# Optimization experiments

Hardware: AMD Instinct MI355X
Metric: run time of the kernel (lower is better)

## Reference

```python
import jax, jax.numpy as jnp
import numpy as np

B, S, D, H = 2, 2048, 1024, 16  # batch, seq, d_model, num_heads
DH = D // H


def setup_inputs() -> dict:
    key = jax.random.key(0)
    ks = jax.random.split(key, 11)
    sc = 1.0 / np.sqrt(D)
    return {
        "q": jax.random.normal(ks[0], (B, S, D), jnp.float32),
        "k": jax.random.normal(ks[1], (B, S, D), jnp.float32),
        "v": jax.random.normal(ks[2], (B, S, D), jnp.float32),
        "wq": jax.random.normal(ks[3], (D, D), jnp.float32) * sc,
        "bq": jax.random.normal(ks[4], (D,), jnp.float32) * 0.01,
        "wk": jax.random.normal(ks[5], (D, D), jnp.float32) * sc,
        "bk": jax.random.normal(ks[6], (D,), jnp.float32) * 0.01,
        "wv": jax.random.normal(ks[7], (D, D), jnp.float32) * sc,
        "bv": jax.random.normal(ks[8], (D,), jnp.float32) * 0.01,
        "wo": jax.random.normal(ks[9], (D, D), jnp.float32) * sc,
        "bo": jax.random.normal(ks[10], (D,), jnp.float32) * 0.01,
    }


def reference(q, k, v, wq, bq, wk, bk, wv, bv, wo, bo):
    # projections: [B,S,D]
    query = q @ wq + bq
    key_ = k @ wk + bk
    value = v @ wv + bv
    # split heads: [B,H,S,DH]
    def split(x):
        return jnp.transpose(x.reshape(B, S, H, DH), (0, 2, 1, 3))
    query, key_, value = split(query), split(key_), split(value)
    # NOTE: original module applies NO 1/sqrt(d_k) scaling
    scores = jnp.einsum("bhqd,bhkd->bhqk", query, key_)
    attn = jax.nn.softmax(scores, axis=-1)
    data = jnp.einsum("bhqk,bhkd->bhqd", attn, value)  # [B,H,S,DH]
    # faithful to original bug: transpose(0,1) then view(B,S,-1)
    data = jnp.swapaxes(data, 0, 1).reshape(B, S, D)
    return data @ wo + bo
```

## Files before the change

kernel.cpp:

```cpp
#include <hip/hip_runtime.h>

typedef _Float16 f16;
typedef _Float16 f16x8 __attribute__((ext_vector_type(8)));
typedef _Float16 f16x4 __attribute__((ext_vector_type(4)));
typedef __fp16   h16x2 __attribute__((ext_vector_type(2)));
typedef float    f32x4 __attribute__((ext_vector_type(4)));

static constexpr int BATCH = 2, SEQ = 2048, DMODEL = 1024, HEADS = 16, DHEAD = 64;
static constexpr int MTOK = BATCH * SEQ;
static constexpr float LOG2E = 1.44269504088896f;

#define GLOBAL_LOAD_LDS16(gptr, lptr)                                              \
  __builtin_amdgcn_global_load_lds(                                                \
      (const __attribute__((address_space(1))) void*)(gptr),                       \
      (__attribute__((address_space(3))) void*)(lptr), 16, 0, 0)

#define MFMA16(a, b, c) __builtin_amdgcn_mfma_f32_16x16x32_f16((a), (b), (c), 0, 0, 0)

#define WAITV_(N) asm volatile("s_waitcnt vmcnt(" #N ")" ::: "memory")
#define WAITV(N) WAITV_(N)

__device__ __forceinline__ float fexp2(float x) {
  float r;
  asm volatile("v_exp_f32 %0, %1" : "=v"(r) : "v"(x));
  return r;
}
__device__ __forceinline__ float m3(float a, float b, float c) {
  return fmaxf(fmaxf(a, b), c);
}

__device__ __forceinline__ int imgAB(int mr, int kr) {
  int pr = mr >> 1;
  int jj = ((mr & 1) << 2) | (kr >> 3);
  int j = jj ^ (pr & 7);
  return pr * 64 + j * 8 + (kr & 7);
}
__device__ __forceinline__ int imgK(int sr, int dh) {
  return sr * 64 + (((dh >> 3) ^ (sr & 7)) << 3) + (dh & 7);
}

__global__ __launch_bounds__(256) void cast3_kernel(
    const float* __restrict__ qs, const float* __restrict__ ks,
    const float* __restrict__ vs, f16* __restrict__ X0, f16* __restrict__ X1,
    f16* __restrict__ X2) {
  const int z = blockIdx.z;
  const float* src = z == 0 ? qs : z == 1 ? ks : vs;
  f16* dst = z == 0 ? X0 : z == 1 ? X1 : X2;
  int c = blockIdx.x * 256 + threadIdx.x;
  int blk = c >> 8, cb = c & 255;
  int pr = cb >> 3, j = cb & 7;
  int jj = j ^ (pr & 7);
  int mr = (pr << 1) | (jj >> 2);
  int kr = (jj & 3) << 3;
  int m = (blk >> 5) * 64 + mr;
  int k = (blk & 31) * 32 + kr;
  const float* s = src + (size_t)m * DMODEL + k;
  f32x4 a = *(const f32x4*)s, b = *(const f32x4*)(s + 4);
  f16x8 o;
  o[0] = (f16)a[0]; o[1] = (f16)a[1]; o[2] = (f16)a[2]; o[3] = (f16)a[3];
  o[4] = (f16)b[0]; o[5] = (f16)b[1]; o[6] = (f16)b[2]; o[7] = (f16)b[3];
  *(f16x8*)(dst + (size_t)c * 8) = o;
}

__global__ __launch_bounds__(256) void transw_kernel(
    const float* __restrict__ w0, const float* __restrict__ w1,
    const float* __restrict__ w2, const float* __restrict__ w3,
    f16* __restrict__ Wimg) {
  const int z = blockIdx.z;
  const float* w = z == 0 ? w0 : z == 1 ? w1 : z == 2 ? w2 : w3;
  f16* t = Wimg + (size_t)z * DMODEL * DMODEL;
  __shared__ f16 lt[64][72];
  const int k0 = blockIdx.x * 64, n0 = blockIdx.y * 64;
  const int r = threadIdx.x >> 2, c0 = (threadIdx.x & 3) * 16;
  const float* src = w + (size_t)(k0 + r) * DMODEL + n0 + c0;
#pragma unroll
  for (int jx = 0; jx < 16; jx += 4) {
    f32x4 x = *(const f32x4*)(src + jx);
    lt[c0 + jx + 0][r] = (f16)x[0];
    lt[c0 + jx + 1][r] = (f16)x[1];
    lt[c0 + jx + 2][r] = (f16)x[2];
    lt[c0 + jx + 3][r] = (f16)x[3];
  }
  __syncthreads();
  const int n = n0 + r;
#pragma unroll
  for (int cw = 0; cw < 2; cw++) {
    int k = k0 + c0 + cw * 8;
    int blk = ((n >> 6) << 5) | (k >> 5);
    int off = blk * 2048 + imgAB(n & 63, k & 31);
    f16x8 v;
#pragma unroll
    for (int e = 0; e < 8; e++) v[e] = lt[r][c0 + cw * 8 + e];
    *(f16x8*)(t + off) = v;
  }
}

__global__ __launch_bounds__(256) void proj_kernel(
    const f16* __restrict__ Ximg, const f16* __restrict__ Wimg,
    const float* __restrict__ bq, const float* __restrict__ bk,
    const float* __restrict__ bv, f16* __restrict__ Qp, f16* __restrict__ Kp,
    f16* __restrict__ Vt, int zbase, size_t aStride) {
  __shared__ f16 As[2][4096];
  __shared__ f16 Bs[2][4096];
  const int z = zbase + blockIdx.z;
  const f16* A = Ximg + (size_t)blockIdx.z * aStride;
  const f16* Bw = Wimg + (size_t)z * DMODEL * DMODEL;
  int lin = blockIdx.x + (blockIdx.y << 3);
  int swz = ((lin & 7) << 5) + (lin >> 3);
  const int n0 = (swz & 7) * 128, m0 = (swz >> 3) * 128;
  const int tid = threadIdx.x, w = tid >> 6, l = tid & 63, q = l & 15, g = l >> 4;
  const int wr = w >> 1, wc = w & 1;
  const int KT = DMODEL >> 5;
  int aoff[4], boff[4];
#pragma unroll
  for (int mi = 0; mi < 4; mi++) {
    int mr = wr * 64 + mi * 16 + q;
    aoff[mi] = ((mr >> 6) << 11) + imgAB(mr & 63, g * 8);
  }
#pragma unroll
  for (int ni = 0; ni < 4; ni++) {
    int nr = wc * 64 + ni * 16 + q;
    boff[ni] = ((nr >> 6) << 11) + imgAB(nr & 63, g * 8);
  }
  f32x4 acc[4][4] = {};

#define PROJ_STAGE(bb, t)                                                          \
  {                                                                                \
    _Pragma("unroll")                                                              \
    for (int i = 0; i < 2; i++) {                                                  \
      int c = w * 2 + i;                                                           \
      size_t ga = (size_t)(((m0 >> 6) + (c >> 2)) * KT + (t)) * 2048 +             \
                  (c & 3) * 512 + l * 8;                                           \
      GLOBAL_LOAD_LDS16(A + ga, (char*)&As[bb][c * 512]);                          \
      size_t gb = (size_t)(((n0 >> 6) + (c >> 2)) * KT + (t)) * 2048 +             \
                  (c & 3) * 512 + l * 8;                                           \
      GLOBAL_LOAD_LDS16(Bw + gb, (char*)&Bs[bb][c * 512]);                         \
    }                                                                              \
  }

  PROJ_STAGE(0, 0);
  for (int t = 0; t < KT; t++) {
    const int bb = t & 1;
    if (t < KT - 1) {
      PROJ_STAGE(bb ^ 1, t + 1);
      WAITV(4);
    } else {
      WAITV(0);
    }
    __builtin_amdgcn_s_barrier();
    f16x8 af[4], bf[4];
#pragma unroll
    for (int mi = 0; mi < 4; mi++) af[mi] = *(const f16x8*)&As[bb][aoff[mi]];
#pragma unroll
    for (int ni = 0; ni < 4; ni++) bf[ni] = *(const f16x8*)&Bs[bb][boff[ni]];
#pragma unroll
    for (int mi = 0; mi < 4; mi++)
#pragma unroll
      for (int ni = 0; ni < 4; ni++)
        acc[mi][ni] = MFMA16(af[mi], bf[ni], acc[mi][ni]);
    __builtin_amdgcn_s_barrier();
  }
  const float* bias = z == 0 ? bq : (z == 1 ? bk : bv);
#pragma unroll
  for (int mi = 0; mi < 4; mi++)
#pragma unroll
    for (int ni = 0; ni < 4; ni++) {
      const int col = n0 + wc * 64 + ni * 16 + q;
      const float bvl = bias[col];
      const int row0 = m0 + wr * 64 + mi * 16 + g * 4;
      if (z == 0) {
#pragma unroll
        for (int r = 0; r < 4; r++)
          Qp[(size_t)(row0 + r) * DMODEL + col] = (f16)((acc[mi][ni][r] + bvl) * LOG2E);
      } else if (z == 1) {
        const int h = col >> 6, dh = col & 63;
#pragma unroll
        for (int r = 0; r < 4; r++) {
          const int row = row0 + r, s = row & (SEQ - 1);
          Kp[(size_t)(((row >> 11) * HEADS + h) * 64 + (s >> 5)) * 2048 + imgK(s & 31, dh)] =
              (f16)(acc[mi][ni][r] + bvl);
        }
      } else {
        const int h = col >> 6, dh = col & 63;
        const int s0 = row0 & (SEQ - 1);
        f16* dst = Vt + (size_t)(((row0 >> 11) * HEADS + h) * 64 + (s0 >> 5)) * 2048 +
                   imgAB(dh, s0 & 31);
        f16x4 ov;
        ov[0] = (f16)(acc[mi][ni][0] + bvl); ov[1] = (f16)(acc[mi][ni][1] + bvl);
        ov[2] = (f16)(acc[mi][ni][2] + bvl); ov[3] = (f16)(acc[mi][ni][3] + bvl);
        *(f16x4*)dst = ov;
      }
    }
}

__global__ __launch_bounds__(128, 2) void attn_kernel(
    const f16* __restrict__ Qp, const f16* __restrict__ Kimg,
    const f16* __restrict__ Vimg, f16* __restrict__ Simg) {
  __shared__ f16 Klds[2][2][2048];
  __shared__ f16 Vlds[2][2][2048];
  __shared__ f16 Plds[2][2][2][512];
  const int tid = threadIdx.x, w = tid >> 6, l = tid & 63, q = l & 15, g = l >> 4;
  const int lin = blockIdx.x;
  const int swz = ((lin & 7) << 7) + (lin >> 3);
  const int qb = swz & 31, bh = swz >> 5;
  const int b = bh >> 4, h = bh & 15;
  const int q0 = qb * 64 + w * 32;

  const f16* qrowA = Qp + (size_t)(b * SEQ + q0 + q) * DMODEL + h * 64;
  const f16x8 qA0 = *(const f16x8*)(qrowA + g * 8);
  const f16x8 qA1 = *(const f16x8*)(qrowA + 32 + g * 8);
  const f16* qrowB = qrowA + (size_t)16 * DMODEL;
  const f16x8 qB0 = *(const f16x8*)(qrowB + g * 8);
  const f16x8 qB1 = *(const f16x8*)(qrowB + 32 + g * 8);

  const f16* kt_base = Kimg + (size_t)(bh * 64) * 2048;
  const f16* vt_base = Vimg + (size_t)(bh * 64) * 2048;

  int koff[4][2];
#pragma unroll
  for (int fn = 0; fn < 4; fn++)
#pragma unroll
    for (int hf = 0; hf < 2; hf++)
      koff[fn][hf] = (fn >> 1) * 2048 + imgK((fn & 1) * 16 + q, hf * 32 + g * 8);
  int voff[4];
#pragma unroll
  for (int fo = 0; fo < 4; fo++) voff[fo] = imgAB(fo * 16 + q, g * 8);
  const int poff = imgAB(q, g * 8);
  int pwoff[2];
  {
    const int pr = q >> 1;
#pragma unroll
    for (int fn = 0; fn < 2; fn++) {
      int jj = ((q & 1) << 2) | (fn * 2 + (g >> 1));
      pwoff[fn] = pr * 64 + ((jj ^ (pr & 7)) << 3) + (g & 1) * 4;
    }
  }
  f16* PwA = &Plds[w][0][0][0];
  f16* PwB = &Plds[w][1][0][0];
  float mA = -1.0e30f, mB = -1.0e30f, lA = 0.f, lB = 0.f;
  f32x4 oA[4] = {}, oB[4] = {};

#define ATTN_STAGE(bb, t)                                                          \
  {                                                                                \
    const f16* sb_ = (w == 0) ? (kt_base + (size_t)(2 * (t)) * 2048)               \
                              : (vt_base + (size_t)(2 * (t)) * 2048);              \
    f16* db_ = (w == 0) ? &Klds[bb][0][0] : &Vlds[bb][0][0];                       \
    _Pragma("unroll")                                                              \
    for (int j_ = 0; j_ < 8; j_++)                                                 \
      GLOBAL_LOAD_LDS16(sb_ + j_ * 512 + l * 8, (char*)(db_ + j_ * 512));          \
  }

#define SOFTMAX_FRAG(s, m_st, l_pt, o, PbF)                                        \
  {                                                                                \
    float lm = fmaxf(m3(m3(s[0][0], s[0][1], s[0][2]),                             \
                        m3(s[0][3], s[1][0], s[1][1]),                             \
                        m3(s[1][2], s[1][3], s[2][0])),                            \
                     m3(m3(s[2][1], s[2][2], s[2][3]),                             \
                        m3(s[3][0], s[3][1], s[3][2]), s[3][3]));                  \
    if (!__all(lm <= m_st + 8.f)) {                                                \
      float mx = fmaxf(lm, __shfl_xor(lm, 16, 64));                                \
      mx = fmaxf(mx, __shfl_xor(mx, 32, 64));                                      \
      const float mnew = fmaxf(m_st, mx);                                          \
      const float sc = fexp2(m_st - mnew);                                         \
      m_st = mnew;                                                                 \
      l_pt *= sc;                                                                  \
      _Pragma("unroll")                                                            \
      for (int fo_ = 0; fo_ < 4; fo_++) {                                          \
        o[fo_][0] *= sc; o[fo_][1] *= sc; o[fo_][2] *= sc; o[fo_][3] *= sc;        \
      }                                                                            \
    }                                                                              \
    float ts = 0.f;                                                                \
    _Pragma("unroll")                                                              \
    for (int fn_ = 0; fn_ < 4; fn_++) {                                            \
      float e0 = fexp2(s[fn_][0] - m_st);                                          \
      float e1 = fexp2(s[fn_][1] - m_st);                                          \
      float e2 = fexp2(s[fn_][2] - m_st);                                          \
      float e3 = fexp2(s[fn_][3] - m_st);                                          \
      ts += (e0 + e1) + (e2 + e3);                                                 \
      union { f16x4 v4; h16x2 h2[2]; } pu_;                                        \
      pu_.h2[0] = __builtin_amdgcn_cvt_pkrtz(e0, e1);                              \
      pu_.h2[1] = __builtin_amdgcn_cvt_pkrtz(e2, e3);                              \
      *(f16x4*)((PbF) + (fn_ >> 1) * 512 + pwoff[fn_ & 1]) = pu_.v4;               \
    }                                                                              \
    l_pt += ts;                                                                    \
  }

  ATTN_STAGE(0, 0);
  for (int t = 0; t < 32; t++) {
    const int bb = t & 1;
    if (t < 31) {
      ATTN_STAGE(bb ^ 1, t + 1);
      WAITV(8);
    } else {
      WAITV(0);
    }
    __builtin_amdgcn_s_barrier();
    const f16* Kb = &Klds[bb][0][0];
    f16x8 kf[4][2];
#pragma unroll
    for (int fn = 0; fn < 4; fn++) {
      kf[fn][0] = *(const f16x8*)(Kb + koff[fn][0]);
      kf[fn][1] = *(const f16x8*)(Kb + koff[fn][1]);
    }
    f32x4 sA[4], sB[4];
    __builtin_amdgcn_s_setprio(1);
#pragma unroll
    for (int fn = 0; fn < 4; fn++) {
      f32x4 z0 = {};
      z0 = MFMA16(kf[fn][0], qA0, z0);
      z0 = MFMA16(kf[fn][1], qA1, z0);
      sA[fn] = z0;
      f32x4 z1 = {};
      z1 = MFMA16(kf[fn][0], qB0, z1);
      z1 = MFMA16(kf[fn][1], qB1, z1);
      sB[fn] = z1;
    }
    __builtin_amdgcn_s_setprio(0);
    SOFTMAX_FRAG(sA, mA, lA, oA, PwA);
    SOFTMAX_FRAG(sB, mB, lB, oB, PwB);
    const f16x8 pA0 = *(const f16x8*)(PwA + poff);
    const f16x8 pA1 = *(const f16x8*)(PwA + 512 + poff);
    const f16x8 pB0 = *(const f16x8*)(PwB + poff);
    const f16x8 pB1 = *(const f16x8*)(PwB + 512 + poff);
    const f16* Vb = &Vlds[bb][0][0];
    f16x8 vf[4][2];
#pragma unroll
    for (int fo = 0; fo < 4; fo++) {
      vf[fo][0] = *(const f16x8*)(Vb + voff[fo]);
      vf[fo][1] = *(const f16x8*)(Vb + 2048 + voff[fo]);
    }
    __builtin_amdgcn_s_setprio(1);
#pragma unroll
    for (int fo = 0; fo < 4; fo++) {
      oA[fo] = MFMA16(vf[fo][0], pA0, oA[fo]);
      oA[fo] = MFMA16(vf[fo][1], pA1, oA[fo]);
      oB[fo] = MFMA16(vf[fo][0], pB0, oB[fo]);
      oB[fo] = MFMA16(vf[fo][1], pB1, oB[fo]);
    }
    __builtin_amdgcn_s_setprio(0);
    __builtin_amdgcn_s_barrier();
  }
  float lsA = lA + __shfl_xor(lA, 16, 64);
  lsA += __shfl_xor(lsA, 32, 64);
  float lsB = lB + __shfl_xor(lB, 16, 64);
  lsB += __shfl_xor(lsB, 32, 64);
  const float invA = 1.f / lsA, invB = 1.f / lsB;
  const int m16 = (2 * h + b) & 15, bp = h >> 3;
#pragma unroll
  for (int half = 0; half < 2; half++) {
    const int s = q0 + half * 16 + q;
    const int tp = bp * SEQ + m16 * 128 + (s >> 4);
    const float inv = half ? invB : invA;
    const f32x4* o = half ? oB : oA;
#pragma unroll
    for (int fo = 0; fo < 4; fo++) {
      const int d0 = (s & 15) * 64 + fo * 16 + g * 4;
      f16* dst = Simg + (size_t)(((tp >> 6) << 5) | (d0 >> 5)) * 2048 + imgAB(tp & 63, d0 & 31);
      f16x4 ov;
      ov[0] = (f16)(o[fo][0] * inv); ov[1] = (f16)(o[fo][1] * inv);
      ov[2] = (f16)(o[fo][2] * inv); ov[3] = (f16)(o[fo][3] * inv);
      *(f16x4*)dst = ov;
    }
  }
}

__global__ __launch_bounds__(256) void ogemm_kernel(
    const f16* __restrict__ Aimg, const f16* __restrict__ Bimg,
    const float* __restrict__ bias, float* __restrict__ out) {
  __shared__ f16 As[2][4096];
  __shared__ f16 Bs[2][2048];
  int lin = blockIdx.x + (blockIdx.y << 4);
  int swz = ((lin & 7) << 6) + (lin >> 3);
  const int n0 = (swz & 15) * 64, m0 = (swz >> 4) * 128;
  const int tid = threadIdx.x, w = tid >> 6, l = tid & 63, q = l & 15, g = l >> 4;
  const int wr = w >> 1, wc = w & 1;
  int aoff[4], boff[2];
#pragma unroll
  for (int mi = 0; mi < 4; mi++) {
    int mr = wr * 64 + mi * 16 + q;
    aoff[mi] = ((mr >> 6) << 11) + imgAB(mr & 63, g * 8);
  }
#pragma unroll
  for (int ni = 0; ni < 2; ni++) boff[ni] = imgAB(wc * 32 + ni * 16 + q, g * 8);
  f32x4 acc[4][2] = {};

#define OG_STAGE(bb, t)                                                            \
  {                                                                                \
    _Pragma("unroll")                                                              \
    for (int i = 0; i < 2; i++) {                                                  \
      int c = w * 2 + i;                                                           \
      size_t ga = (size_t)(((m0 >> 6) + (c >> 2)) * 32 + (t)) * 2048 +             \
                  (c & 3) * 512 + l * 8;                                           \
      GLOBAL_LOAD_LDS16(Aimg + ga, (char*)&As[bb][c * 512]);                       \
    }                                                                              \
    size_t gb = (size_t)((n0 >> 6) * 32 + (t)) * 2048 + w * 512 + l * 8;           \
    GLOBAL_LOAD_LDS16(Bimg + gb, (char*)&Bs[bb][w * 512]);                         \
  }

  OG_STAGE(0, 0);
  for (int t = 0; t < 32; t++) {
    const int bb = t & 1;
    if (t < 31) {
      OG_STAGE(bb ^ 1, t + 1);
      WAITV(3);
    } else {
      WAITV(0);
    }
    __builtin_amdgcn_s_barrier();
    f16x8 af[4], bf[2];
#pragma unroll
    for (int mi = 0; mi < 4; mi++) af[mi] = *(const f16x8*)&As[bb][aoff[mi]];
#pragma unroll
    for (int ni = 0; ni < 2; ni++) bf[ni] = *(const f16x8*)&Bs[bb][boff[ni]];
#pragma unroll
    for (int mi = 0; mi < 4; mi++)
#pragma unroll
      for (int ni = 0; ni < 2; ni++)
        acc[mi][ni] = MFMA16(af[mi], bf[ni], acc[mi][ni]);
    __builtin_amdgcn_s_barrier();
  }
#pragma unroll
  for (int mi = 0; mi < 4; mi++)
#pragma unroll
    for (int ni = 0; ni < 2; ni++) {
      const int col = n0 + wc * 32 + ni * 16 + q;
      const float bvl = bias[col];
      const int row0 = m0 + wr * 64 + mi * 16 + g * 4;
#pragma unroll
      for (int r = 0; r < 4; r++)
        out[(size_t)(row0 + r) * DMODEL + col] = acc[mi][ni][r] + bvl;
    }
}

extern "C" void kernel_launch(void* const* d_in, const int* in_sizes, int n_in,
                              void* d_out, int out_size, void* d_ws, size_t ws_size,
                              hipStream_t stream) {
  const float* q  = (const float*)d_in[0];
  const float* k  = (const float*)d_in[1];
  const float* v  = (const float*)d_in[2];
  const float* wq = (const float*)d_in[3];
  const float* bq = (const float*)d_in[4];
  const float* wk = (const float*)d_in[5];
  const float* bk = (const float*)d_in[6];
  const float* wv = (const float*)d_in[7];
  const float* bv = (const float*)d_in[8];
  const float* wo = (const float*)d_in[9];
  const float* bo = (const float*)d_in[10];

  const size_t XSZ = (size_t)MTOK * DMODEL;
  f16* ws = (f16*)d_ws;
  const bool fused = ws_size >= (56ull << 20);

  f16 *X0, *X1, *X2, *Qp, *Kp, *Vt, *Wimg, *scr;
  if (fused) {
    X0 = ws; X1 = ws + XSZ; X2 = ws + 2 * XSZ;
    Qp = ws + 3 * XSZ; Kp = ws + 4 * XSZ; Vt = ws + 5 * XSZ;
    Wimg = ws + 6 * XSZ;
    scr = X0;
  } else {
    X0 = X1 = X2 = ws;
    Qp = ws + XSZ; Kp = ws + 2 * XSZ; Vt = ws + 3 * XSZ;
    Wimg = ws + 4 * XSZ;
    scr = X0;
  }

  dim3 blk(256), blk128(128);
  dim3 gT(16, 16, 4);
  dim3 gA(1024);
  dim3 gO(16, 32);

  transw_kernel<<<gT, blk, 0, stream>>>(wq, wk, wv, wo, Wimg);

  if (fused) {
    cast3_kernel<<<dim3(2048, 1, 3), blk, 0, stream>>>(q, k, v, X0, X1, X2);
    proj_kernel<<<dim3(8, 32, 3), blk, 0, stream>>>(X0, Wimg, bq, bk, bv, Qp, Kp, Vt, 0, XSZ);
  } else {
    cast3_kernel<<<dim3(2048, 1, 1), blk, 0, stream>>>(q, q, q, X0, X0, X0);
    proj_kernel<<<dim3(8, 32, 1), blk, 0, stream>>>(X0, Wimg, bq, bk, bv, Qp, Kp, Vt, 0, 0);
    cast3_kernel<<<dim3(2048, 1, 1), blk, 0, stream>>>(k, k, k, X0, X0, X0);
    proj_kernel<<<dim3(8, 32, 1), blk, 0, stream>>>(X0, Wimg, bq, bk, bv, Qp, Kp, Vt, 1, 0);
    cast3_kernel<<<dim3(2048, 1, 1), blk, 0, stream>>>(v, v, v, X0, X0, X0);
    proj_kernel<<<dim3(8, 32, 1), blk, 0, stream>>>(X0, Wimg, bq, bk, bv, Qp, Kp, Vt, 2, 0);
  }

  attn_kernel<<<gA, blk128, 0, stream>>>(Qp, Kp, Vt, scr);
  ogemm_kernel<<<gO, blk, 0, stream>>>(scr, Wimg + (size_t)3 * DMODEL * DMODEL, bo, (float*)d_out);
}
```

Before: 235.9 us.

## Triple-buffer GEMM tile loads and compute softmax row sums via MFMA

The projection and output GEMM kernels move from double to triple-buffered LDS staging, prefetching two k-tiles ahead with adjusted vmcnt waits and rotating buffer pointers. This hides more global-load latency at the cost of extra LDS per block, which may lower occupancy. The attention kernel no longer sums softmax probabilities with scalar adds and final cross-lane shuffles. Instead it accumulates row sums by multiplying a ones vector against the fp16 P fragments with extra MFMAs, so the sums use the rounded fp16 values.

```diff
diff --git a/kernel.cpp b/kernel.cpp
--- a/kernel.cpp
+++ b/kernel.cpp
@@ -100,8 +100,8 @@
     const float* __restrict__ bq, const float* __restrict__ bk,
     const float* __restrict__ bv, f16* __restrict__ Qp, f16* __restrict__ Kp,
     f16* __restrict__ Vt, int zbase, size_t aStride) {
-  __shared__ f16 As[2][4096];
-  __shared__ f16 Bs[2][4096];
+  __shared__ f16 As[3][4096];
+  __shared__ f16 Bs[3][4096];
   const int z = zbase + blockIdx.z;
   const f16* A = Ximg + (size_t)blockIdx.z * aStride;
   const f16* Bw = Wimg + (size_t)z * DMODEL * DMODEL;
@@ -123,26 +123,30 @@
     boff[ni] = ((nr >> 6) << 11) + imgAB(nr & 63, g * 8);
   }
   f32x4 acc[4][4] = {};
-
-#define PROJ_STAGE(bb, t)                                                          \
+  f16 *pa0 = &As[0][0], *pa1 = &As[1][0], *pa2 = &As[2][0];
+  f16 *pb0 = &Bs[0][0], *pb1 = &Bs[1][0], *pb2 = &Bs[2][0];
+
+#define PROJ_STAGE(abuf, bbuf, t)                                                  \
   {                                                                                \
     _Pragma("unroll")                                                              \
     for (int i = 0; i < 2; i++) {                                                  \
       int c = w * 2 + i;                                                           \
       size_t ga = (size_t)(((m0 >> 6) + (c >> 2)) * KT + (t)) * 2048 +             \
                   (c & 3) * 512 + l * 8;                                           \
-      GLOBAL_LOAD_LDS16(A + ga, (char*)&As[bb][c * 512]);                          \
+      GLOBAL_LOAD_LDS16(A + ga, (char*)&(abuf)[c * 512]);                          \
       size_t gb = (size_t)(((n0 >> 6) + (c >> 2)) * KT + (t)) * 2048 +             \
                   (c & 3) * 512 + l * 8;                                           \
-      GLOBAL_LOAD_LDS16(Bw + gb, (char*)&Bs[bb][c * 512]);                         \
+      GLOBAL_LOAD_LDS16(Bw + gb, (char*)&(bbuf)[c * 512]);                         \
     }                                                                              \
   }
 
-  PROJ_STAGE(0, 0);
+  PROJ_STAGE(pa0, pb0, 0);
+  PROJ_STAGE(pa1, pb1, 1);
   for (int t = 0; t < KT; t++) {
-    const int bb = t & 1;
-    if (t < KT - 1) {
-      PROJ_STAGE(bb ^ 1, t + 1);
+    if (t + 2 < KT) {
+      PROJ_STAGE(pa2, pb2, t + 2);
+      WAITV(8);
+    } else if (t + 1 < KT) {
       WAITV(4);
     } else {
       WAITV(0);
@@ -150,15 +154,17 @@
     __builtin_amdgcn_s_barrier();
     f16x8 af[4], bf[4];
 #pragma unroll
-    for (int mi = 0; mi < 4; mi++) af[mi] = *(const f16x8*)&As[bb][aoff[mi]];
-#pragma unroll
-    for (int ni = 0; ni < 4; ni++) bf[ni] = *(const f16x8*)&Bs[bb][boff[ni]];
+    for (int mi = 0; mi < 4; mi++) af[mi] = *(const f16x8*)&pa0[aoff[mi]];
+#pragma unroll
+    for (int ni = 0; ni < 4; ni++) bf[ni] = *(const f16x8*)&pb0[boff[ni]];
 #pragma unroll
     for (int mi = 0; mi < 4; mi++)
 #pragma unroll
       for (int ni = 0; ni < 4; ni++)
         acc[mi][ni] = MFMA16(af[mi], bf[ni], acc[mi][ni]);
     __builtin_amdgcn_s_barrier();
+    f16* tA = pa0; pa0 = pa1; pa1 = pa2; pa2 = tA;
+    f16* tB = pb0; pb0 = pb1; pb1 = pb2; pb2 = tB;
   }
   const float* bias = z == 0 ? bq : (z == 1 ? bk : bv);
 #pragma unroll
@@ -237,8 +243,12 @@
   }
   f16* PwA = &Plds[w][0][0][0];
   f16* PwB = &Plds[w][1][0][0];
-  float mA = -1.0e30f, mB = -1.0e30f, lA = 0.f, lB = 0.f;
+  float mA = -1.0e30f, mB = -1.0e30f;
   f32x4 oA[4] = {}, oB[4] = {};
+  f32x4 lAa = {}, lBa = {};
+  f16x8 ones;
+#pragma unroll
+  for (int e = 0; e < 8; e++) ones[e] = (f16)1.0f;
 
 #define ATTN_STAGE(bb, t)                                                          \
   {                                                                                \
@@ -250,7 +260,7 @@
       GLOBAL_LOAD_LDS16(sb_ + j_ * 512 + l * 8, (char*)(db_ + j_ * 512));          \
   }
 
-#define SOFTMAX_FRAG(s, m_st, l_pt, o, PbF)                                        \
+#define SOFTMAX_FRAG(s, m_st, l_acc, o, PbF)                                       \
   {                                                                                \
     float lm = fmaxf(m3(m3(s[0][0], s[0][1], s[0][2]),                             \
                         m3(s[0][3], s[1][0], s[1][1]),                             \
@@ -263,26 +273,23 @@
       const float mnew = fmaxf(m_st, mx);                                          \
       const float sc = fexp2(m_st - mnew);                                         \
       m_st = mnew;                                                                 \
-      l_pt *= sc;                                                                  \
+      l_acc[0] *= sc; l_acc[1] *= sc; l_acc[2] *= sc; l_acc[3] *= sc;              \
       _Pragma("unroll")                                                            \
       for (int fo_ = 0; fo_ < 4; fo_++) {                                          \
         o[fo_][0] *= sc; o[fo_][1] *= sc; o[fo_][2] *= sc; o[fo_][3] *= sc;        \
       }                                                                            \
     }                                                                              \
-    float ts = 0.f;                                                                \
     _Pragma("unroll")                                                              \
     for (int fn_ = 0; fn_ < 4; fn_++) {                                            \
       float e0 = fexp2(s[fn_][0] - m_st);                                          \
       float e1 = fexp2(s[fn_][1] - m_st);                                          \
       float e2 = fexp2(s[fn_][2] - m_st);                                          \
       float e3 = fexp2(s[fn_][3] - m_st);                                          \
-      ts += (e0 + e1) + (e2 + e3);                                                 \
       union { f16x4 v4; h16x2 h2[2]; } pu_;                                        \
       pu_.h2[0] = __builtin_amdgcn_cvt_pkrtz(e0, e1);                              \
       pu_.h2[1] = __builtin_amdgcn_cvt_pkrtz(e2, e3);                              \
       *(f16x4*)((PbF) + (fn_ >> 1) * 512 + pwoff[fn_ & 1]) = pu_.v4;               \
     }                                                                              \
-    l_pt += ts;                                                                    \
   }
 
   ATTN_STAGE(0, 0);
@@ -316,8 +323,8 @@
       sB[fn] = z1;
     }
     __builtin_amdgcn_s_setprio(0);
-    SOFTMAX_FRAG(sA, mA, lA, oA, PwA);
-    SOFTMAX_FRAG(sB, mB, lB, oB, PwB);
+    SOFTMAX_FRAG(sA, mA, lAa, oA, PwA);
+    SOFTMAX_FRAG(sB, mB, lBa, oB, PwB);
     const f16x8 pA0 = *(const f16x8*)(PwA + poff);
     const f16x8 pA1 = *(const f16x8*)(PwA + 512 + poff);
     const f16x8 pB0 = *(const f16x8*)(PwB + poff);
@@ -337,14 +344,14 @@
       oB[fo] = MFMA16(vf[fo][0], pB0, oB[fo]);
       oB[fo] = MFMA16(vf[fo][1], pB1, oB[fo]);
     }
+    lAa = MFMA16(ones, pA0, lAa);
+    lAa = MFMA16(ones, pA1, lAa);
+    lBa = MFMA16(ones, pB0, lBa);
+    lBa = MFMA16(ones, pB1, lBa);
     __builtin_amdgcn_s_setprio(0);
     __builtin_amdgcn_s_barrier();
   }
-  float lsA = lA + __shfl_xor(lA, 16, 64);
-  lsA += __shfl_xor(lsA, 32, 64);
-  float lsB = lB + __shfl_xor(lB, 16, 64);
-  lsB += __shfl_xor(lsB, 32, 64);
-  const float invA = 1.f / lsA, invB = 1.f / lsB;
+  const float invA = 1.f / lAa[0], invB = 1.f / lBa[0];
   const int m16 = (2 * h + b) & 15, bp = h >> 3;
 #pragma unroll
   for (int half = 0; half < 2; half++) {
@@ -367,8 +374,8 @@
 __global__ __launch_bounds__(256) void ogemm_kernel(
     const f16* __restrict__ Aimg, const f16* __restrict__ Bimg,
     const float* __restrict__ bias, float* __restrict__ out) {
-  __shared__ f16 As[2][4096];
-  __shared__ f16 Bs[2][2048];
+  __shared__ f16 As[3][4096];
+  __shared__ f16 Bs[3][2048];
   int lin = blockIdx.x + (blockIdx.y << 4);
   int swz = ((lin & 7) << 6) + (lin >> 3);
   const int n0 = (swz & 15) * 64, m0 = (swz >> 4) * 128;
@@ -383,25 +390,29 @@
 #pragma unroll
   for (int ni = 0; ni < 2; ni++) boff[ni] = imgAB(wc * 32 + ni * 16 + q, g * 8);
   f32x4 acc[4][2] = {};
-
-#define OG_STAGE(bb, t)                                                            \
+  f16 *pa0 = &As[0][0], *pa1 = &As[1][0], *pa2 = &As[2][0];
+  f16 *pb0 = &Bs[0][0], *pb1 = &Bs[1][0], *pb2 = &Bs[2][0];
+
+#define OG_STAGE(abuf, bbuf, t)                                                    \
   {                                                                                \
     _Pragma("unroll")                                                              \
     for (int i = 0; i < 2; i++) {                                                  \
       int c = w * 2 + i;                                                           \
       size_t ga = (size_t)(((m0 >> 6) + (c >> 2)) * 32 + (t)) * 2048 +             \
                   (c & 3) * 512 + l * 8;                                           \
-      GLOBAL_LOAD_LDS16(Aimg + ga, (char*)&As[bb][c * 512]);                       \
+      GLOBAL_LOAD_LDS16(Aimg + ga, (char*)&(abuf)[c * 512]);                       \
     }                                                                              \
     size_t gb = (size_t)((n0 >> 6) * 32 + (t)) * 2048 + w * 512 + l * 8;           \
-    GLOBAL_LOAD_LDS16(Bimg + gb, (char*)&Bs[bb][w * 512]);                         \
-  }
-
-  OG_STAGE(0, 0);
+    GLOBAL_LOAD_LDS16(Bimg + gb, (char*)&(bbuf)[w * 512]);                         \
+  }
+
+  OG_STAGE(pa0, pb0, 0);
+  OG_STAGE(pa1, pb1, 1);
   for (int t = 0; t < 32; t++) {
-    const int bb = t & 1;
-    if (t < 31) {
-      OG_STAGE(bb ^ 1, t + 1);
+    if (t + 2 < 32) {
+      OG_STAGE(pa2, pb2, t + 2);
+      WAITV(6);
+    } else if (t + 1 < 32) {
       WAITV(3);
     } else {
       WAITV(0);
@@ -409,15 +420,17 @@
     __builtin_amdgcn_s_barrier();
     f16x8 af[4], bf[2];
 #pragma unroll
-    for (int mi = 0; mi < 4; mi++) af[mi] = *(const f16x8*)&As[bb][aoff[mi]];
-#pragma unroll
-    for (int ni = 0; ni < 2; ni++) bf[ni] = *(const f16x8*)&Bs[bb][boff[ni]];
+    for (int mi = 0; mi < 4; mi++) af[mi] = *(const f16x8*)&pa0[aoff[mi]];
+#pragma unroll
+    for (int ni = 0; ni < 2; ni++) bf[ni] = *(const f16x8*)&pb0[boff[ni]];
 #pragma unroll
     for (int mi = 0; mi < 4; mi++)
 #pragma unroll
       for (int ni = 0; ni < 2; ni++)
         acc[mi][ni] = MFMA16(af[mi], bf[ni], acc[mi][ni]);
     __builtin_amdgcn_s_barrier();
+    f16* tA = pa0; pa0 = pa1; pa1 = pa2; pa2 = tA;
+    f16* tB = pb0; pb0 = pb1; pb1 = pb2; pb2 = tB;
   }
 #pragma unroll
   for (int mi = 0; mi < 4; mi++)
```

Measured after the change: 240.0 us. No clear change (+1.7%).
